# Optimization experiments

Measured on AMD Instinct MI355X. Metric: run time of the kernel, lower is better.

## Reference

```python
import jax, jax.numpy as jnp
import numpy as np

N_NODES = 100000
N_EDGES = 1600000
NFEAT, NHID, NCLASS = 512, 128, 64


def setup_inputs() -> dict:
    key = jax.random.key(0)
    ks = jax.random.split(key, 8)
    y = jax.random.normal(ks[0], (N_NODES, NFEAT), dtype=jnp.float32)
    src = jax.random.randint(ks[1], (N_EDGES,), 0, N_NODES, dtype=jnp.int64)
    dst = jax.random.randint(ks[2], (N_EDGES,), 0, N_NODES, dtype=jnp.int64)
    edge_w = jax.random.uniform(ks[3], (N_EDGES,), dtype=jnp.float32)
    # GraphConvolution params (Glorot-ish scale)
    W1 = jax.random.normal(ks[4], (NFEAT, NHID), dtype=jnp.float32) / np.sqrt(NFEAT)
    b1 = jax.random.normal(ks[5], (NHID,), dtype=jnp.float32) * 0.01
    W2 = jax.random.normal(ks[6], (NHID, NCLASS), dtype=jnp.float32) / np.sqrt(NHID)
    b2 = jax.random.normal(ks[7], (NCLASS,), dtype=jnp.float32) * 0.01
    return {"y": y, "src": src, "dst": dst, "edge_w": edge_w,
            "W1": W1, "b1": b1, "W2": W2, "b2": b2}


def _graph_conv(x, W, b, src, dst, edge_w, n_nodes):
    # support = x @ W ; out = spmm(adj, support) + b  (adj in COO form)
    support = x @ W                                   # [N, out_dim]
    msgs = support[src] * edge_w[:, None]             # [E, out_dim] gather
    agg = jax.ops.segment_sum(msgs, dst, num_segments=n_nodes)  # scatter-add
    return agg + b


def reference(y, src, dst, edge_w, W1, b1, W2, b2):
    h = jax.nn.leaky_relu(_graph_conv(y, W1, b1, src, dst, edge_w, N_NODES),
                          negative_slope=0.01)        # F.leaky_relu default
    y_embedding = h
    logits = _graph_conv(h, W2, b2, src, dst, edge_w, N_NODES)
    return (jax.nn.softmax(logits, axis=1), y_embedding)
```

## Files before the change

### kernel.cpp

```cpp
#include <hip/hip_runtime.h>
#include <hip/hip_fp16.h>

#define NN 100000
#define NE 1600000
#define F0 512
#define F1 128
#define F2 64

typedef short bf16x8 __attribute__((ext_vector_type(8)));
typedef float f32x4  __attribute__((ext_vector_type(4)));

static __device__ __forceinline__ unsigned short f2bf(float f) {
    unsigned int u = __float_as_uint(f);
    return (unsigned short)((u + 0x7FFFu + ((u >> 16) & 1u)) >> 16);
}

static __device__ __forceinline__ unsigned short f2h(float f) {
    __half h = __float2half(f);
    return *(unsigned short*)&h;
}

static __device__ __forceinline__ float2 h2f2(unsigned int u) {
    __half2 h = *(__half2*)&u;
    return __half22float2(h);
}

__global__ __launch_bounds__(256)
void wt_kernel(const float* __restrict__ W1, const float* __restrict__ W2,
               unsigned short* __restrict__ W1t, unsigned short* __restrict__ W2t)
{
    int i = blockIdx.x * 256 + threadIdx.x;
    if (i < F0 * F1) {
        int n = i / F0, k = i % F0;
        W1t[i] = f2bf(W1[k * F1 + n]);
    } else {
        int j = i - F0 * F1;
        if (j < F1 * F2) {
            int n = j / F1, k = j % F1;
            W2t[j] = f2bf(W2[k * F2 + n]);
        }
    }
}

template<int BM, int BN, int BK, int TN>
__global__ __launch_bounds__(256)
void mfma_gemm(const float* __restrict__ A, const unsigned short* __restrict__ Bt,
               unsigned short* __restrict__ C, int M, int K, int N)
{
    constexpr int LDA = BK + 8;
    constexpr int LDB = BK + 8;
    __shared__ unsigned short As[BM * LDA];
    __shared__ unsigned short Bs[BN * LDB];

    const int tid  = threadIdx.x;
    const int wave = tid >> 6;
    const int lane = tid & 63;
    const int lr   = lane & 15;
    const int quad = lane >> 4;
    const int row0 = blockIdx.x * BM;

    f32x4 acc[2][TN];
#pragma unroll
    for (int i = 0; i < 2; i++)
#pragma unroll
        for (int j = 0; j < TN; j++) acc[i][j] = (f32x4)0.f;

    for (int k0 = 0; k0 < K; k0 += BK) {
#pragma unroll
        for (int l = tid; l < BM * (BK / 4); l += 256) {
            int m  = l / (BK / 4);
            int kq = l % (BK / 4);
            int rg = row0 + m; if (rg >= M) rg = M - 1;
            float4 v = *(const float4*)(A + (long long)rg * K + k0 + kq * 4);
            ushort4 b = make_ushort4(f2bf(v.x), f2bf(v.y), f2bf(v.z), f2bf(v.w));
            *(ushort4*)(&As[m * LDA + kq * 4]) = b;
        }
#pragma unroll
        for (int l = tid; l < BN * (BK / 8); l += 256) {
            int n  = l / (BK / 8);
            int ko = l % (BK / 8);
            uint4 v = *(const uint4*)(Bt + (long long)n * K + k0 + ko * 8);
            *(uint4*)(&Bs[n * LDB + ko * 8]) = v;
        }
        __syncthreads();

#pragma unroll
        for (int kk = 0; kk < BK; kk += 32) {
            bf16x8 a[2], b[TN];
#pragma unroll
            for (int tm = 0; tm < 2; tm++)
                a[tm] = *(const bf16x8*)(&As[(wave * 32 + tm * 16 + lr) * LDA + kk + quad * 8]);
#pragma unroll
            for (int tn = 0; tn < TN; tn++)
                b[tn] = *(const bf16x8*)(&Bs[(tn * 16 + lr) * LDB + kk + quad * 8]);
#pragma unroll
            for (int tm = 0; tm < 2; tm++)
#pragma unroll
                for (int tn = 0; tn < TN; tn++)
                    acc[tm][tn] = __builtin_amdgcn_mfma_f32_16x16x32_bf16(
                        a[tm], b[tn], acc[tm][tn], 0, 0, 0);
        }
        __syncthreads();
    }

#pragma unroll
    for (int tm = 0; tm < 2; tm++) {
#pragma unroll
        for (int r = 0; r < 4; r++) {
            int row = row0 + wave * 32 + tm * 16 + quad * 4 + r;
            if (row < M) {
#pragma unroll
                for (int tn = 0; tn < TN; tn++)
                    C[(long long)row * N + tn * 16 + lr] = f2h(acc[tm][tn][r]);
            }
        }
    }
}

__global__ __launch_bounds__(256)
void hist_kernel(const int* __restrict__ dst, int* __restrict__ cnt,
                 int* __restrict__ rank, int ne)
{
    int e = blockIdx.x * 256 + threadIdx.x;
    if (e < ne) rank[e] = atomicAdd(&cnt[dst[e]], 1);
}

__global__ __launch_bounds__(256)
void scan1_kernel(const int* __restrict__ cnt, int* __restrict__ rowptr,
                  int* __restrict__ bsum, int n)
{
    __shared__ int s[256];
    int t = threadIdx.x;
    int i = blockIdx.x * 256 + t;
    int v = (i < n) ? cnt[i] : 0;
    s[t] = v;
    __syncthreads();
#pragma unroll
    for (int off = 1; off < 256; off <<= 1) {
        int x = (t >= off) ? s[t - off] : 0;
        __syncthreads();
        s[t] += x;
        __syncthreads();
    }
    if (i < n) rowptr[i] = s[t] - v;
    if (t == 255) bsum[blockIdx.x] = s[255];
}

__global__ __launch_bounds__(512)
void scan2_kernel(int* __restrict__ bsum, int nb, int* __restrict__ rowptr, int n, int ne)
{
    __shared__ int s[512];
    int t = threadIdx.x;
    int v = (t < nb) ? bsum[t] : 0;
    s[t] = v;
    __syncthreads();
#pragma unroll
    for (int off = 1; off < 512; off <<= 1) {
        int x = (t >= off) ? s[t - off] : 0;
        __syncthreads();
        s[t] += x;
        __syncthreads();
    }
    if (t < nb) bsum[t] = s[t] - v;
    if (t == 0) rowptr[n] = ne;
}

__global__ __launch_bounds__(256)
void scan3_kernel(int* __restrict__ rowptr, const int* __restrict__ bsum, int n)
{
    int i = blockIdx.x * 256 + threadIdx.x;
    if (i < n) rowptr[i] += bsum[i >> 8];
}

__global__ __launch_bounds__(256)
void fill_kernel(const int* __restrict__ src, const int* __restrict__ dst,
                 const float* __restrict__ ew, const int* __restrict__ rowptr,
                 const int* __restrict__ rank, int2* __restrict__ rec, int ne)
{
    int e = blockIdx.x * 256 + threadIdx.x;
    if (e >= ne) return;
    int d = dst[e];
    int pos = rowptr[d] + rank[e];
    rec[pos] = make_int2(src[e], __float_as_int(ew[e]));
}

__global__ __launch_bounds__(256)
void agg1_fused_kernel(const unsigned int* __restrict__ sup, const int2* __restrict__ rec,
                       const int* __restrict__ rowptr, const float2* __restrict__ b1,
                       const unsigned short* __restrict__ W2t,
                       float2* __restrict__ h, unsigned short* __restrict__ sup2, int n)
{
    constexpr int LDH = F1 + 8;
    __shared__ unsigned short hsb[16 * LDH];

    const int tid  = threadIdx.x;
    const int w    = tid >> 6;
    const int lane = tid & 63;
    const int base = blockIdx.x * 16;

    float2 bb = b1[lane];

#pragma unroll
    for (int i = 0; i < 4; i++) {
        int row  = w * 4 + i;
        int node = base + row;
        float2 acc = make_float2(0.f, 0.f);
        if (node < n) {
            int j   = rowptr[node];
            int end = rowptr[node + 1];
            for (; j + 4 <= end; j += 4) {
                int2 r0 = rec[j];
                int2 r1 = rec[j + 1];
                int2 r2 = rec[j + 2];
                int2 r3 = rec[j + 3];
                unsigned int u0 = sup[(long long)r0.x * 64 + lane];
                unsigned int u1 = sup[(long long)r1.x * 64 + lane];
                unsigned int u2 = sup[(long long)r2.x * 64 + lane];
                unsigned int u3 = sup[(long long)r3.x * 64 + lane];
                float w0 = __int_as_float(r0.y);
                float w1 = __int_as_float(r1.y);
                float w2 = __int_as_float(r2.y);
                float w3 = __int_as_float(r3.y);
                float2 f0 = h2f2(u0);
                float2 f1 = h2f2(u1);
                float2 f2 = h2f2(u2);
                float2 f3 = h2f2(u3);
                acc.x = fmaf(f0.x, w0, acc.x);  acc.y = fmaf(f0.y, w0, acc.y);
                acc.x = fmaf(f1.x, w1, acc.x);  acc.y = fmaf(f1.y, w1, acc.y);
                acc.x = fmaf(f2.x, w2, acc.x);  acc.y = fmaf(f2.y, w2, acc.y);
                acc.x = fmaf(f3.x, w3, acc.x);  acc.y = fmaf(f3.y, w3, acc.y);
            }
            for (; j < end; j++) {
                int2 r0 = rec[j];
                unsigned int u0 = sup[(long long)r0.x * 64 + lane];
                float w0 = __int_as_float(r0.y);
                float2 f0 = h2f2(u0);
                acc.x = fmaf(f0.x, w0, acc.x);
                acc.y = fmaf(f0.y, w0, acc.y);
            }
            acc.x += bb.x;
            acc.y += bb.y;
            acc.x = acc.x > 0.f ? acc.x : 0.01f * acc.x;
            acc.y = acc.y > 0.f ? acc.y : 0.01f * acc.y;
            h[(long long)node * 64 + lane] = acc;
        }
        ushort2 hv = (node < n) ? make_ushort2(f2bf(acc.x), f2bf(acc.y))
                                : make_ushort2(0, 0);
        *(ushort2*)(&hsb[row * LDH + lane * 2]) = hv;
    }
    __syncthreads();

    const int lr   = lane & 15;
    const int quad = lane >> 4;
    f32x4 acc2 = (f32x4)0.f;
#pragma unroll
    for (int kk = 0; kk < F1; kk += 32) {
        bf16x8 a = *(const bf16x8*)(&hsb[lr * LDH + kk + quad * 8]);
        bf16x8 b = *(const bf16x8*)(W2t + (w * 16 + lr) * F1 + kk + quad * 8);
        acc2 = __builtin_amdgcn_mfma_f32_16x16x32_bf16(a, b, acc2, 0, 0, 0);
    }
#pragma unroll
    for (int r = 0; r < 4; r++) {
        int node = base + quad * 4 + r;
        if (node < n)
            sup2[(long long)node * 64 + w * 16 + lr] = f2h(acc2[r]);
    }
}

__global__ __launch_bounds__(256)
void agg2_kernel(const unsigned short* __restrict__ sup, const int2* __restrict__ rec,
                 const int* __restrict__ rowptr, const float* __restrict__ b2,
                 float* __restrict__ out, int n)
{
    int node = blockIdx.x * 4 + (threadIdx.x >> 6);
    int lane = threadIdx.x & 63;
    if (node >= n) return;

    int j   = rowptr[node];
    int end = rowptr[node + 1];
    float acc = 0.f;

    for (; j + 4 <= end; j += 4) {
        int2 r0 = rec[j];
        int2 r1 = rec[j + 1];
        int2 r2 = rec[j + 2];
        int2 r3 = rec[j + 3];
        unsigned short u0 = sup[(long long)r0.x * 64 + lane];
        unsigned short u1 = sup[(long long)r1.x * 64 + lane];
        unsigned short u2 = sup[(long long)r2.x * 64 + lane];
        unsigned short u3 = sup[(long long)r3.x * 64 + lane];
        acc = fmaf(__half2float(*(__half*)&u0), __int_as_float(r0.y), acc);
        acc = fmaf(__half2float(*(__half*)&u1), __int_as_float(r1.y), acc);
        acc = fmaf(__half2float(*(__half*)&u2), __int_as_float(r2.y), acc);
        acc = fmaf(__half2float(*(__half*)&u3), __int_as_float(r3.y), acc);
    }
    for (; j < end; j++) {
        int2 r0 = rec[j];
        unsigned short u0 = sup[(long long)r0.x * 64 + lane];
        acc = fmaf(__half2float(*(__half*)&u0), __int_as_float(r0.y), acc);
    }

    float v = acc + b2[lane];
    float m = v;
#pragma unroll
    for (int off = 32; off; off >>= 1) m = fmaxf(m, __shfl_xor(m, off, 64));
    float e = __expf(v - m);
    float s = e;
#pragma unroll
    for (int off = 32; off; off >>= 1) s += __shfl_xor(s, off, 64);
    out[(long long)node * 64 + lane] = e / s;
}

extern "C" void kernel_launch(void* const* d_in, const int* in_sizes, int n_in,
                              void* d_out, int out_size, void* d_ws, size_t ws_size,
                              hipStream_t stream)
{
    const float* y   = (const float*)d_in[0];
    const int*   src = (const int*)  d_in[1];
    const int*   dst = (const int*)  d_in[2];
    const float* ew  = (const float*)d_in[3];
    const float* W1  = (const float*)d_in[4];
    const float* b1  = (const float*)d_in[5];
    const float* W2  = (const float*)d_in[6];
    const float* b2  = (const float*)d_in[7];

    float* out     = (float*)d_out;
    float* softout = out;
    float* h       = out + (size_t)NN * F2;

    char* ws = (char*)d_ws;
    size_t o = 0;
    auto alloc = [&](size_t bytes) -> void* {
        void* p = ws + o;
        o = (o + bytes + 255) & ~(size_t)255;
        return p;
    };
    unsigned short* sup  = (unsigned short*)alloc((size_t)NN * F1 * 2);
    unsigned short* sup2 = (unsigned short*)alloc((size_t)NN * F2 * 2);
    int2*           rec  = (int2*)          alloc((size_t)NE * 8);
    int*            rank = (int*)           alloc((size_t)NE * 4);
    int*            rowptr = (int*)         alloc((size_t)(NN + 2) * 4);
    int*            cnt  = (int*)           alloc((size_t)NN * 4);
    int*            bsum = (int*)           alloc(512 * 4);
    unsigned short* W1t  = (unsigned short*)alloc((size_t)F0 * F1 * 2);
    unsigned short* W2t  = (unsigned short*)alloc((size_t)F1 * F2 * 2);

    const int NB = (NN + 255) / 256;

    wt_kernel<<<(F0 * F1 + F1 * F2 + 255) / 256, 256, 0, stream>>>(W1, W2, W1t, W2t);

    hipMemsetAsync(cnt, 0, (size_t)NN * 4, stream);
    hist_kernel<<<(NE + 255) / 256, 256, 0, stream>>>(dst, cnt, rank, NE);
    scan1_kernel<<<NB, 256, 0, stream>>>(cnt, rowptr, bsum, NN);
    scan2_kernel<<<1, 512, 0, stream>>>(bsum, NB, rowptr, NN, NE);
    scan3_kernel<<<NB, 256, 0, stream>>>(rowptr, bsum, NN);
    fill_kernel<<<(NE + 255) / 256, 256, 0, stream>>>(src, dst, ew, rowptr, rank, rec, NE);

    mfma_gemm<128, 128, 64, 8>
        <<<(NN + 127) / 128, 256, 0, stream>>>(y, W1t, sup, NN, F0, F1);

    agg1_fused_kernel<<<(NN + 15) / 16, 256, 0, stream>>>(
        (const unsigned int*)sup, rec, rowptr, (const float2*)b1, W2t,
        (float2*)h, sup2, NN);

    agg2_kernel<<<(NN + 3) / 4, 256, 0, stream>>>(
        sup2, rec, rowptr, b2, softout, NN);
}
```

Before: 612.7 us.

## Overlap GEMM halves with edge histogram and CSR fill; unroll gathers by eight

The first-layer GEMM is split into two halves. Each half is launched in the same grid as the edge histogram or the CSR fill blocks, so the compute-bound matrix work overlaps the atomic-heavy, memory-bound edge passes and two launches go away. The aggregation loops now unroll by eight with separate load phases, so more independent gathers are in flight. The fused grids raise shared-memory and register pressure for the edge blocks, and larger unrolls add registers and tail handling.

```diff
diff --git a/kernel.cpp b/kernel.cpp
--- a/kernel.cpp
+++ b/kernel.cpp
@@ -42,22 +42,41 @@
     }
 }
 
-template<int BM, int BN, int BK, int TN>
-__global__ __launch_bounds__(256)
-void mfma_gemm(const float* __restrict__ A, const unsigned short* __restrict__ Bt,
-               unsigned short* __restrict__ C, int M, int K, int N)
+template<int BM, int BN, int BK, int TN, bool FILL>
+__global__ __launch_bounds__(256)
+void gemm_edge_kernel(const float* __restrict__ A, const unsigned short* __restrict__ Bt,
+                      unsigned short* __restrict__ C, int M, int K, int N,
+                      int row_base, int gemm_blocks,
+                      const int* __restrict__ src, const int* __restrict__ dst,
+                      const float* __restrict__ ew, const int* __restrict__ rowptr,
+                      int* __restrict__ cnt, int* __restrict__ rank,
+                      int2* __restrict__ rec, int ne)
 {
     constexpr int LDA = BK + 8;
     constexpr int LDB = BK + 8;
     __shared__ unsigned short As[BM * LDA];
     __shared__ unsigned short Bs[BN * LDB];
+
+    if ((int)blockIdx.x >= gemm_blocks) {
+        int e = ((int)blockIdx.x - gemm_blocks) * 256 + threadIdx.x;
+        if (e < ne) {
+            if constexpr (!FILL) {
+                rank[e] = atomicAdd(&cnt[dst[e]], 1);
+            } else {
+                int d = dst[e];
+                int pos = rowptr[d] + rank[e];
+                rec[pos] = make_int2(src[e], __float_as_int(ew[e]));
+            }
+        }
+        return;
+    }
 
     const int tid  = threadIdx.x;
     const int wave = tid >> 6;
     const int lane = tid & 63;
     const int lr   = lane & 15;
     const int quad = lane >> 4;
-    const int row0 = blockIdx.x * BM;
+    const int row0 = row_base + (int)blockIdx.x * BM;
 
     f32x4 acc[2][TN];
 #pragma unroll
@@ -118,14 +137,6 @@
 }
 
 __global__ __launch_bounds__(256)
-void hist_kernel(const int* __restrict__ dst, int* __restrict__ cnt,
-                 int* __restrict__ rank, int ne)
-{
-    int e = blockIdx.x * 256 + threadIdx.x;
-    if (e < ne) rank[e] = atomicAdd(&cnt[dst[e]], 1);
-}
-
-__global__ __launch_bounds__(256)
 void scan1_kernel(const int* __restrict__ cnt, int* __restrict__ rowptr,
                   int* __restrict__ bsum, int n)
 {
@@ -170,18 +181,6 @@
 {
     int i = blockIdx.x * 256 + threadIdx.x;
     if (i < n) rowptr[i] += bsum[i >> 8];
-}
-
-__global__ __launch_bounds__(256)
-void fill_kernel(const int* __restrict__ src, const int* __restrict__ dst,
-                 const float* __restrict__ ew, const int* __restrict__ rowptr,
-                 const int* __restrict__ rank, int2* __restrict__ rec, int ne)
-{
-    int e = blockIdx.x * 256 + threadIdx.x;
-    if (e >= ne) return;
-    int d = dst[e];
-    int pos = rowptr[d] + rank[e];
-    rec[pos] = make_int2(src[e], __float_as_int(ew[e]));
 }
 
 __global__ __launch_bounds__(256)
@@ -208,33 +207,39 @@
         if (node < n) {
             int j   = rowptr[node];
             int end = rowptr[node + 1];
-            for (; j + 4 <= end; j += 4) {
+            for (; j + 8 <= end; j += 8) {
+                int2 r[8];
+#pragma unroll
+                for (int u = 0; u < 8; u++) r[u] = rec[j + u];
+                unsigned int uu[8];
+#pragma unroll
+                for (int u = 0; u < 8; u++)
+                    uu[u] = sup[(long long)r[u].x * 64 + lane];
+#pragma unroll
+                for (int u = 0; u < 8; u++) {
+                    float2 f = h2f2(uu[u]);
+                    float  ww = __int_as_float(r[u].y);
+                    acc.x = fmaf(f.x, ww, acc.x);
+                    acc.y = fmaf(f.y, ww, acc.y);
+                }
+            }
+            for (; j + 2 <= end; j += 2) {
                 int2 r0 = rec[j];
                 int2 r1 = rec[j + 1];
-                int2 r2 = rec[j + 2];
-                int2 r3 = rec[j + 3];
                 unsigned int u0 = sup[(long long)r0.x * 64 + lane];
                 unsigned int u1 = sup[(long long)r1.x * 64 + lane];
-                unsigned int u2 = sup[(long long)r2.x * 64 + lane];
-                unsigned int u3 = sup[(long long)r3.x * 64 + lane];
+                float2 f0 = h2f2(u0);
+                float2 f1 = h2f2(u1);
                 float w0 = __int_as_float(r0.y);
                 float w1 = __int_as_float(r1.y);
-                float w2 = __int_as_float(r2.y);
-                float w3 = __int_as_float(r3.y);
-                float2 f0 = h2f2(u0);
-                float2 f1 = h2f2(u1);
-                float2 f2 = h2f2(u2);
-                float2 f3 = h2f2(u3);
                 acc.x = fmaf(f0.x, w0, acc.x);  acc.y = fmaf(f0.y, w0, acc.y);
                 acc.x = fmaf(f1.x, w1, acc.x);  acc.y = fmaf(f1.y, w1, acc.y);
-                acc.x = fmaf(f2.x, w2, acc.x);  acc.y = fmaf(f2.y, w2, acc.y);
-                acc.x = fmaf(f3.x, w3, acc.x);  acc.y = fmaf(f3.y, w3, acc.y);
-            }
-            for (; j < end; j++) {
+            }
+            if (j < end) {
                 int2 r0 = rec[j];
                 unsigned int u0 = sup[(long long)r0.x * 64 + lane];
+                float2 f0 = h2f2(u0);
                 float w0 = __int_as_float(r0.y);
-                float2 f0 = h2f2(u0);
                 acc.x = fmaf(f0.x, w0, acc.x);
                 acc.y = fmaf(f0.y, w0, acc.y);
             }
@@ -280,21 +285,27 @@
     int end = rowptr[node + 1];
     float acc = 0.f;
 
-    for (; j + 4 <= end; j += 4) {
+    for (; j + 8 <= end; j += 8) {
+        int2 r[8];
+#pragma unroll
+        for (int u = 0; u < 8; u++) r[u] = rec[j + u];
+        unsigned short uu[8];
+#pragma unroll
+        for (int u = 0; u < 8; u++)
+            uu[u] = sup[(long long)r[u].x * 64 + lane];
+#pragma unroll
+        for (int u = 0; u < 8; u++)
+            acc = fmaf(__half2float(*(__half*)&uu[u]), __int_as_float(r[u].y), acc);
+    }
+    for (; j + 2 <= end; j += 2) {
         int2 r0 = rec[j];
         int2 r1 = rec[j + 1];
-        int2 r2 = rec[j + 2];
-        int2 r3 = rec[j + 3];
         unsigned short u0 = sup[(long long)r0.x * 64 + lane];
         unsigned short u1 = sup[(long long)r1.x * 64 + lane];
-        unsigned short u2 = sup[(long long)r2.x * 64 + lane];
-        unsigned short u3 = sup[(long long)r3.x * 64 + lane];
         acc = fmaf(__half2float(*(__half*)&u0), __int_as_float(r0.y), acc);
         acc = fmaf(__half2float(*(__half*)&u1), __int_as_float(r1.y), acc);
-        acc = fmaf(__half2float(*(__half*)&u2), __int_as_float(r2.y), acc);
-        acc = fmaf(__half2float(*(__half*)&u3), __int_as_float(r3.y), acc);
-    }
-    for (; j < end; j++) {
+    }
+    if (j < end) {
         int2 r0 = rec[j];
         unsigned short u0 = sup[(long long)r0.x * 64 + lane];
         acc = fmaf(__half2float(*(__half*)&u0), __int_as_float(r0.y), acc);
@@ -346,18 +357,24 @@
     unsigned short* W2t  = (unsigned short*)alloc((size_t)F1 * F2 * 2);
 
     const int NB = (NN + 255) / 256;
-
+    const int GB = (NN + 127) / 128;
+    const int GA = GB / 2;
+    const int EB = (NE + 255) / 256;
+
+    hipMemsetAsync(cnt, 0, (size_t)NN * 4, stream);
     wt_kernel<<<(F0 * F1 + F1 * F2 + 255) / 256, 256, 0, stream>>>(W1, W2, W1t, W2t);
 
-    hipMemsetAsync(cnt, 0, (size_t)NN * 4, stream);
-    hist_kernel<<<(NE + 255) / 256, 256, 0, stream>>>(dst, cnt, rank, NE);
+    gemm_edge_kernel<128, 128, 64, 8, false><<<GA + EB, 256, 0, stream>>>(
+        y, W1t, sup, NN, F0, F1, 0, GA,
+        src, dst, ew, rowptr, cnt, rank, rec, NE);
+
     scan1_kernel<<<NB, 256, 0, stream>>>(cnt, rowptr, bsum, NN);
     scan2_kernel<<<1, 512, 0, stream>>>(bsum, NB, rowptr, NN, NE);
     scan3_kernel<<<NB, 256, 0, stream>>>(rowptr, bsum, NN);
-    fill_kernel<<<(NE + 255) / 256, 256, 0, stream>>>(src, dst, ew, rowptr, rank, rec, NE);
-
-    mfma_gemm<128, 128, 64, 8>
-        <<<(NN + 127) / 128, 256, 0, stream>>>(y, W1t, sup, NN, F0, F1);
+
+    gemm_edge_kernel<128, 128, 64, 8, true><<<(GB - GA) + EB, 256, 0, stream>>>(
+        y, W1t, sup, NN, F0, F1, GA * 128, GB - GA,
+        src, dst, ew, rowptr, cnt, rank, rec, NE);
 
     agg1_fused_kernel<<<(NN + 15) / 16, 256, 0, stream>>>(
         (const unsigned int*)sup, rec, rowptr, (const float2*)b1, W2t,
```

New measurement: 570.9 us. 1.07x faster.
